# Performance work log

Hardware: AMD Instinct MI355X
Metric: run time of the kernel (lower is better)

Reference implementation:

```python
import jax, jax.numpy as jnp
import numpy as np

O, G, GS = 8192, 64, 128   # out_features, n_groups, group_size
I = G * GS                 # in_features = 8192
RANK = 128                 # svd_rank
RESULT_SHAPE = (O, I)


def setup_inputs() -> dict:
    key = jax.random.key(0)
    k1, k2, k3, k4, k5 = jax.random.split(key, 5)
    weight = jax.random.randint(k1, (O, G, GS), 0, 256, dtype=jnp.int32)
    # realistic small per-group scales and zero points
    scale = jax.random.uniform(k2, (O, G, 1), dtype=jnp.float32) * 0.01 + 1e-4
    zero_point = jax.random.normal(k3, (O, G, 1), dtype=jnp.float32) * 0.05
    svd_up = jax.random.normal(k4, (O, RANK), dtype=jnp.float32) * 0.02
    svd_down = jax.random.normal(k5, (RANK, I), dtype=jnp.float32) * 0.02
    return {
        "weight": weight,
        "scale": scale,
        "zero_point": zero_point,
        "svd_up": svd_up,
        "svd_down": svd_down,
    }


def reference(weight, scale, zero_point, svd_up, svd_down):
    # addcmul: zero_point + weight * scale  (broadcast over group dim)
    result = zero_point + weight.astype(scale.dtype) * scale      # [O, G, GS]
    result = result.reshape(RESULT_SHAPE)                          # [O, I]
    # low-rank SVD correction: result += svd_up @ svd_down (addmm_)
    result = result + jnp.matmul(svd_up, svd_down)                 # [O, I]
    return result.astype(jnp.float32)                              # final dtype cast
```

## Files before the change

kernel.cpp:

```cpp
#include <hip/hip_runtime.h>
#include <hip/hip_bf16.h>

#define O_DIM 8192
#define I_DIM 8192
#define G_DIM 64
#define RANK  128

typedef __bf16 bf16x8 __attribute__((ext_vector_type(8)));
typedef __bf16 bf16x4 __attribute__((ext_vector_type(4)));
typedef float  f32x4  __attribute__((ext_vector_type(4)));
typedef int    i32x4  __attribute__((ext_vector_type(4)));

__global__ void k_convert_up(const float* __restrict__ up, __bf16* __restrict__ A_bf) {
    size_t t = (size_t)blockIdx.x * blockDim.x + threadIdx.x;
    const float4* in4 = (const float4*)up;
    float4 v = in4[t];
    bf16x4 o = { (__bf16)v.x, (__bf16)v.y, (__bf16)v.z, (__bf16)v.w };
    *(bf16x4*)(A_bf + 4 * t) = o;
}

__global__ void k_transpose_down(const float* __restrict__ down, __bf16* __restrict__ Bt) {
    __shared__ __bf16 tile[64][132];
    int tid = threadIdx.x;
    int ib  = blockIdx.x * 64;
    int il  = tid & 63;
    int k4  = tid >> 6;
    for (int kk = 0; kk < 32; ++kk) {
        int k = kk * 4 + k4;
        tile[il][k] = (__bf16)down[(size_t)k * I_DIM + ib + il];
    }
    __syncthreads();
    uint2* dst = (uint2*)(Bt + (size_t)ib * RANK);
    #pragma unroll
    for (int jj = 0; jj < 8; ++jj) {
        int f   = (jj * 256 + tid) * 4;
        int i_l = f >> 7;
        int k_l = f & 127;
        dst[jj * 256 + tid] = *(const uint2*)&tile[i_l][k_l];
    }
}

__global__ __launch_bounds__(256, 2)
void k_main(const int* __restrict__ weight, const float* __restrict__ scale,
            const float* __restrict__ zp, const __bf16* __restrict__ A_bf,
            const __bf16* __restrict__ Bt_bf, float* __restrict__ out) {
    int tid = threadIdx.x;
    int g       = blockIdx.x;
    int rowbase = blockIdx.y * 128;
    int colbase = g * 128;

    int w    = tid >> 6;
    int lane = tid & 63;
    int l15  = lane & 15;
    int quad = lane >> 4;
    int wrow = (w >> 1) * 64;
    int wcol = (w & 1) * 64;

    const __bf16* Ap = A_bf  + (size_t)(rowbase + wrow + l15) * RANK + quad * 8;
    const __bf16* Bp = Bt_bf + (size_t)(colbase + wcol + l15) * RANK + quad * 8;

    bf16x8 af[2][4], bfr[2][4];
    #pragma unroll
    for (int j = 0; j < 2; ++j)
        #pragma unroll
        for (int rb = 0; rb < 4; ++rb) {
            af[j][rb]  = *(const bf16x8*)(Ap + rb * 16 * RANK + j * 32);
            bfr[j][rb] = *(const bf16x8*)(Bp + rb * 16 * RANK + j * 32);
        }
    __builtin_amdgcn_sched_barrier(0);

    float sv[4], zv[4];
    #pragma unroll
    for (int rb = 0; rb < 4; ++rb) {
        int row = rowbase + wrow + rb * 16 + l15;
        sv[rb] = scale[(size_t)row * G_DIM + g];
        zv[rb] = zp[(size_t)row * G_DIM + g];
    }
    __builtin_amdgcn_sched_barrier(0);

    i32x4 wt[4][4];
    const int* Wp = weight + (size_t)(rowbase + wrow + l15) * I_DIM
                  + colbase + wcol + quad * 4;
    #pragma unroll
    for (int rb = 0; rb < 4; ++rb)
        #pragma unroll
        for (int cb = 0; cb < 4; ++cb)
            wt[rb][cb] = *(const i32x4*)(Wp + (size_t)(rb * 16) * I_DIM + cb * 16);
    __builtin_amdgcn_sched_barrier(0);

    f32x4 acc[4][4];
    #pragma unroll
    for (int rb = 0; rb < 4; ++rb)
        #pragma unroll
        for (int cb = 0; cb < 4; ++cb)
            acc[rb][cb] = (f32x4){0.f, 0.f, 0.f, 0.f};

    #pragma unroll
    for (int j = 0; j < 2; ++j)
        #pragma unroll
        for (int rb = 0; rb < 4; ++rb)
            #pragma unroll
            for (int cb = 0; cb < 4; ++cb)
                acc[rb][cb] = __builtin_amdgcn_mfma_f32_16x16x32_bf16(
                    bfr[j][cb], af[j][rb], acc[rb][cb], 0, 0, 0);
    __builtin_amdgcn_sched_barrier(0);

    #pragma unroll
    for (int j = 0; j < 2; ++j)
        #pragma unroll
        for (int rb = 0; rb < 4; ++rb) {
            af[j][rb]  = *(const bf16x8*)(Ap + rb * 16 * RANK + (2 + j) * 32);
            bfr[j][rb] = *(const bf16x8*)(Bp + rb * 16 * RANK + (2 + j) * 32);
        }
    __builtin_amdgcn_sched_barrier(0);

    #pragma unroll
    for (int j = 0; j < 2; ++j)
        #pragma unroll
        for (int rb = 0; rb < 4; ++rb)
            #pragma unroll
            for (int cb = 0; cb < 4; ++cb)
                acc[rb][cb] = __builtin_amdgcn_mfma_f32_16x16x32_bf16(
                    bfr[j][cb], af[j][rb], acc[rb][cb], 0, 0, 0);
    __builtin_amdgcn_sched_barrier(0);

    size_t obase = (size_t)(rowbase + wrow + l15) * I_DIM + colbase + wcol + quad * 4;
    #pragma unroll
    for (int rb = 0; rb < 4; ++rb) {
        float s = sv[rb];
        float z = zv[rb];
        #pragma unroll
        for (int cb = 0; cb < 4; ++cb) {
            f32x4 v;
            #pragma unroll
            for (int e = 0; e < 4; ++e)
                v[e] = fmaf((float)wt[rb][cb][e], s, z) + acc[rb][cb][e];
            *(f32x4*)(out + obase + (size_t)(rb * 16) * I_DIM + cb * 16) = v;
        }
    }
}

extern "C" void kernel_launch(void* const* d_in, const int* in_sizes, int n_in,
                              void* d_out, int out_size, void* d_ws, size_t ws_size,
                              hipStream_t stream) {
    const int*   weight = (const int*)d_in[0];
    const float* scale  = (const float*)d_in[1];
    const float* zp     = (const float*)d_in[2];
    const float* up     = (const float*)d_in[3];
    const float* down   = (const float*)d_in[4];
    float* out = (float*)d_out;

    __bf16* A_bf  = (__bf16*)d_ws;
    __bf16* Bt_bf = A_bf + (size_t)O_DIM * RANK;

    k_convert_up<<<1024, 256, 0, stream>>>(up, A_bf);
    k_transpose_down<<<128, 256, 0, stream>>>(down, Bt_bf);

    dim3 grid(64, 64);
    k_main<<<grid, 256, 0, stream>>>(weight, scale, zp, A_bf, Bt_bf, out);
}
```

Before: 482.8 us.

## Restructure main kernel into persistent row-strip loop with weight prefetch

The main kernel now launches 512 blocks, each owning a 16-row strip, with each wave walking 2048 columns in 64-column chunks. Instead of one-shot 128x128 tiles, it double-buffers the int32 weight loads across chunks, reloads the B fragments per chunk, and uses nontemporal stores for the output. The goal is to keep loads in flight over a long loop and to avoid the output stream polluting the cache. In exchange, B fragments are re-read from cache by every row strip and there are fewer waves in flight per CU.

Measured after the change: 570.5 us. 18.2% more time.

```diff
diff --git a/kernel.cpp b/kernel.cpp
--- a/kernel.cpp
+++ b/kernel.cpp
@@ -44,98 +44,108 @@
 void k_main(const int* __restrict__ weight, const float* __restrict__ scale,
             const float* __restrict__ zp, const __bf16* __restrict__ A_bf,
             const __bf16* __restrict__ Bt_bf, float* __restrict__ out) {
-    int tid = threadIdx.x;
-    int g       = blockIdx.x;
-    int rowbase = blockIdx.y * 128;
-    int colbase = g * 128;
-
+    int tid  = threadIdx.x;
     int w    = tid >> 6;
     int lane = tid & 63;
     int l15  = lane & 15;
     int quad = lane >> 4;
-    int wrow = (w >> 1) * 64;
-    int wcol = (w & 1) * 64;
 
-    const __bf16* Ap = A_bf  + (size_t)(rowbase + wrow + l15) * RANK + quad * 8;
-    const __bf16* Bp = Bt_bf + (size_t)(colbase + wcol + l15) * RANK + quad * 8;
+    int rowbase = blockIdx.x * 16;
+    int wcb     = w * 2048;
+    int row     = rowbase + l15;
 
-    bf16x8 af[2][4], bfr[2][4];
+    const __bf16* Ap = A_bf + (size_t)row * RANK + quad * 8;
+    bf16x8 af[4];
     #pragma unroll
-    for (int j = 0; j < 2; ++j)
-        #pragma unroll
-        for (int rb = 0; rb < 4; ++rb) {
-            af[j][rb]  = *(const bf16x8*)(Ap + rb * 16 * RANK + j * 32);
-            bfr[j][rb] = *(const bf16x8*)(Bp + rb * 16 * RANK + j * 32);
-        }
+    for (int kc = 0; kc < 4; ++kc)
+        af[kc] = *(const bf16x8*)(Ap + kc * 32);
+
+    const int*    Wp    = weight + (size_t)row * I_DIM + wcb + quad * 4;
+    float*        Op    = out    + (size_t)row * I_DIM + wcb + quad * 4;
+    const __bf16* Bbase = Bt_bf  + (size_t)(wcb + l15) * RANK + quad * 8;
+    const float*  Sp    = scale  + (size_t)row * G_DIM + (wcb >> 7);
+    const float*  Zp    = zp     + (size_t)row * G_DIM + (wcb >> 7);
+
+    i32x4 wtA[4], wtB[4];
+    #pragma unroll
+    for (int nb = 0; nb < 4; ++nb)
+        wtA[nb] = *(const i32x4*)(Wp + nb * 16);
     __builtin_amdgcn_sched_barrier(0);
 
-    float sv[4], zv[4];
-    #pragma unroll
-    for (int rb = 0; rb < 4; ++rb) {
-        int row = rowbase + wrow + rb * 16 + l15;
-        sv[rb] = scale[(size_t)row * G_DIM + g];
-        zv[rb] = zp[(size_t)row * G_DIM + g];
-    }
-    __builtin_amdgcn_sched_barrier(0);
+    #pragma unroll 1
+    for (int gi = 0; gi < 16; ++gi) {
+        float sv = Sp[gi];
+        float zv = Zp[gi];
 
-    i32x4 wt[4][4];
-    const int* Wp = weight + (size_t)(rowbase + wrow + l15) * I_DIM
-                  + colbase + wcol + quad * 4;
-    #pragma unroll
-    for (int rb = 0; rb < 4; ++rb)
-        #pragma unroll
-        for (int cb = 0; cb < 4; ++cb)
-            wt[rb][cb] = *(const i32x4*)(Wp + (size_t)(rb * 16) * I_DIM + cb * 16);
-    __builtin_amdgcn_sched_barrier(0);
+        {
+            int c = 2 * gi;
+            const __bf16* Bc = Bbase + (size_t)c * 64 * RANK;
+            bf16x8 bfr[4][4];
+            #pragma unroll
+            for (int nb = 0; nb < 4; ++nb)
+                #pragma unroll
+                for (int kc = 0; kc < 4; ++kc)
+                    bfr[nb][kc] = *(const bf16x8*)(Bc + (size_t)nb * 16 * RANK + kc * 32);
+            __builtin_amdgcn_sched_barrier(0);
+            #pragma unroll
+            for (int nb = 0; nb < 4; ++nb)
+                wtB[nb] = *(const i32x4*)(Wp + (c + 1) * 64 + nb * 16);
+            __builtin_amdgcn_sched_barrier(0);
 
-    f32x4 acc[4][4];
-    #pragma unroll
-    for (int rb = 0; rb < 4; ++rb)
-        #pragma unroll
-        for (int cb = 0; cb < 4; ++cb)
-            acc[rb][cb] = (f32x4){0.f, 0.f, 0.f, 0.f};
+            f32x4 acc[4];
+            #pragma unroll
+            for (int nb = 0; nb < 4; ++nb) acc[nb] = (f32x4){0.f, 0.f, 0.f, 0.f};
+            #pragma unroll
+            for (int kc = 0; kc < 4; ++kc)
+                #pragma unroll
+                for (int nb = 0; nb < 4; ++nb)
+                    acc[nb] = __builtin_amdgcn_mfma_f32_16x16x32_bf16(
+                        bfr[nb][kc], af[kc], acc[nb], 0, 0, 0);
 
-    #pragma unroll
-    for (int j = 0; j < 2; ++j)
-        #pragma unroll
-        for (int rb = 0; rb < 4; ++rb)
             #pragma unroll
-            for (int cb = 0; cb < 4; ++cb)
-                acc[rb][cb] = __builtin_amdgcn_mfma_f32_16x16x32_bf16(
-                    bfr[j][cb], af[j][rb], acc[rb][cb], 0, 0, 0);
-    __builtin_amdgcn_sched_barrier(0);
+            for (int nb = 0; nb < 4; ++nb) {
+                f32x4 v;
+                #pragma unroll
+                for (int e = 0; e < 4; ++e)
+                    v[e] = fmaf((float)wtA[nb][e], sv, zv) + acc[nb][e];
+                __builtin_nontemporal_store(v, (f32x4*)(Op + c * 64 + nb * 16));
+            }
+        }
 
-    #pragma unroll
-    for (int j = 0; j < 2; ++j)
-        #pragma unroll
-        for (int rb = 0; rb < 4; ++rb) {
-            af[j][rb]  = *(const bf16x8*)(Ap + rb * 16 * RANK + (2 + j) * 32);
-            bfr[j][rb] = *(const bf16x8*)(Bp + rb * 16 * RANK + (2 + j) * 32);
-        }
-    __builtin_amdgcn_sched_barrier(0);
+        {
+            int c = 2 * gi + 1;
+            int pf = (c < 31) ? (c + 1) : 31;
+            const __bf16* Bc = Bbase + (size_t)c * 64 * RANK;
+            bf16x8 bfr[4][4];
+            #pragma unroll
+            for (int nb = 0; nb < 4; ++nb)
+                #pragma unroll
+                for (int kc = 0; kc < 4; ++kc)
+                    bfr[nb][kc] = *(const bf16x8*)(Bc + (size_t)nb * 16 * RANK + kc * 32);
+            __builtin_amdgcn_sched_barrier(0);
+            #pragma unroll
+            for (int nb = 0; nb < 4; ++nb)
+                wtA[nb] = *(const i32x4*)(Wp + pf * 64 + nb * 16);
+            __builtin_amdgcn_sched_barrier(0);
 
-    #pragma unroll
-    for (int j = 0; j < 2; ++j)
-        #pragma unroll
-        for (int rb = 0; rb < 4; ++rb)
+            f32x4 acc[4];
             #pragma unroll
-            for (int cb = 0; cb < 4; ++cb)
-                acc[rb][cb] = __builtin_amdgcn_mfma_f32_16x16x32_bf16(
-                    bfr[j][cb], af[j][rb], acc[rb][cb], 0, 0, 0);
-    __builtin_amdgcn_sched_barrier(0);
+            for (int nb = 0; nb < 4; ++nb) acc[nb] = (f32x4){0.f, 0.f, 0.f, 0.f};
+            #pragma unroll
+            for (int kc = 0; kc < 4; ++kc)
+                #pragma unroll
+                for (int nb = 0; nb < 4; ++nb)
+                    acc[nb] = __builtin_amdgcn_mfma_f32_16x16x32_bf16(
+                        bfr[nb][kc], af[kc], acc[nb], 0, 0, 0);
 
-    size_t obase = (size_t)(rowbase + wrow + l15) * I_DIM + colbase + wcol + quad * 4;
-    #pragma unroll
-    for (int rb = 0; rb < 4; ++rb) {
-        float s = sv[rb];
-        float z = zv[rb];
-        #pragma unroll
-        for (int cb = 0; cb < 4; ++cb) {
-            f32x4 v;
             #pragma unroll
-            for (int e = 0; e < 4; ++e)
-                v[e] = fmaf((float)wt[rb][cb][e], s, z) + acc[rb][cb][e];
-            *(f32x4*)(out + obase + (size_t)(rb * 16) * I_DIM + cb * 16) = v;
+            for (int nb = 0; nb < 4; ++nb) {
+                f32x4 v;
+                #pragma unroll
+                for (int e = 0; e < 4; ++e)
+                    v[e] = fmaf((float)wtB[nb][e], sv, zv) + acc[nb][e];
+                __builtin_nontemporal_store(v, (f32x4*)(Op + c * 64 + nb * 16));
+            }
         }
     }
 }
@@ -156,6 +166,5 @@
     k_convert_up<<<1024, 256, 0, stream>>>(up, A_bf);
     k_transpose_down<<<128, 256, 0, stream>>>(down, Bt_bf);
 
-    dim3 grid(64, 64);
-    k_main<<<grid, 256, 0, stream>>>(weight, scale, zp, A_bf, Bt_bf, out);
+    k_main<<<512, 256, 0, stream>>>(weight, scale, zp, A_bf, Bt_bf, out);
 }
```
